# Optimization experiments

Hardware: AMD Instinct MI355X
Metric: run time of the kernel (lower is better)

## Reference

```python
import jax, jax.numpy as jnp
import numpy as np

Q_DIM = 256; KV_DIM = 256; C = 32; N_HEAD = 8; OUT_DIM = 256
B1, B2, LQ, LK = 1, 128, 256, 256


def _glorot(key, shape, gain=1.0):
    fan_in, fan_out = shape[-2], shape[-1]
    std = gain * np.sqrt(2.0 / float(fan_in + fan_out))
    dev = np.sqrt(3.0) * std
    return jax.random.uniform(key, shape, jnp.float32, -dev, dev)


def setup_inputs() -> dict:
    key = jax.random.key(0)
    ks = jax.random.split(key, 12)
    q_data = jax.random.normal(ks[0], (B1, B2, LQ, Q_DIM), jnp.float32)
    kv_data = jax.random.normal(ks[1], (B1, B2, LK, KV_DIM), jnp.float32)
    bias = jax.random.normal(ks[2], (B1, B2, N_HEAD, LQ, LK), jnp.float32)
    nonbatched_bias = jax.random.normal(ks[3], (B1, N_HEAD, LQ, LK), jnp.float32)
    # torch Linear weights are [out, in]; original init is zeros but we use
    # glorot for a non-degenerate numerical baseline.
    Wq = _glorot(ks[4], (N_HEAD * C, Q_DIM))
    Wk = _glorot(ks[5], (N_HEAD * C, KV_DIM))
    Wv = _glorot(ks[6], (N_HEAD * C, KV_DIM))
    Wg = _glorot(ks[7], (N_HEAD * C, Q_DIM))
    bg = jnp.ones((N_HEAD * C,), jnp.float32)  # bias_init=1.0
    Wo = _glorot(ks[8], (OUT_DIM, N_HEAD * C))
    bo = jnp.zeros((OUT_DIM,), jnp.float32)
    return dict(q_data=q_data, kv_data=kv_data, bias=bias,
                nonbatched_bias=nonbatched_bias, Wq=Wq, Wk=Wk, Wv=Wv,
                Wg=Wg, bg=bg, Wo=Wo, bo=bo)


def reference(q_data, kv_data, bias, nonbatched_bias, Wq, Wk, Wv, Wg, bg, Wo, bo):
    c = C
    # projections: [b1,b2,len,n_head,c]
    q = (q_data @ Wq.T).reshape(*q_data.shape[:-1], N_HEAD, c) * (c ** -0.5)
    k = (kv_data @ Wk.T).reshape(*kv_data.shape[:-1], N_HEAD, c)
    v = (kv_data @ Wv.T).reshape(*kv_data.shape[:-1], N_HEAD, c)
    # logits: [b1,b2,n_head,len_q,len_kv]
    logits = jnp.einsum('bsqhc,bskhc->bshqk', q, k)
    logits = logits + bias + nonbatched_bias[:, None]
    weights = jax.nn.softmax(logits, axis=-1)
    weighted_avg = jnp.einsum('bshqk,bskhc->bsqhc', weights, v)
    gate = jax.nn.sigmoid((q_data @ Wg.T + bg).reshape(*q_data.shape[:-1], N_HEAD, c))
    weighted_avg = weighted_avg * gate
    out = weighted_avg.reshape(*weighted_avg.shape[:-2], N_HEAD * c) @ Wo.T + bo
    return out
```

## Files before the change

kernel.cpp:

```cpp
#include <hip/hip_runtime.h>
#include <hip/hip_bf16.h>

#define NB2 128
#define LQK 256
#define DIM 256
#define NH 8
#define CC 32

typedef __bf16 bf16x8 __attribute__((ext_vector_type(8)));
typedef __bf16 bf16x4 __attribute__((ext_vector_type(4)));
typedef __bf16 bf16x2 __attribute__((ext_vector_type(2)));
typedef float f32x4 __attribute__((ext_vector_type(4)));

#define MFMA16 __builtin_amdgcn_mfma_f32_16x16x32_bf16

#define TP 72

#define NTOK ((size_t)NB2 * LQK * NH * CC)

static __device__ __forceinline__ void gload_lds16(const void* g, void* l) {
    __builtin_amdgcn_global_load_lds(
        (const __attribute__((address_space(1))) unsigned int*)g,
        (__attribute__((address_space(3))) unsigned int*)l,
        16, 0, 0);
}

__global__ __launch_bounds__(256) void k_cvt(
    const float* __restrict__ qd, const float* __restrict__ kvd,
    const float* __restrict__ Wq, const float* __restrict__ Wk,
    const float* __restrict__ Wv, const float* __restrict__ Wg,
    const float* __restrict__ Wo,
    __bf16* __restrict__ qbf, __bf16* __restrict__ kvbf,
    __bf16* __restrict__ wBF)
{
    const int b = blockIdx.x;
    if (b < 8192) {
        size_t i = ((size_t)b * 256 + threadIdx.x) * 8;
        const float* src;
        __bf16* dst;
        if (i < NTOK) { src = qd + i; dst = qbf + i; }
        else          { src = kvd + (i - NTOK); dst = kvbf + (i - NTOK); }
        f32x4 a = *(const f32x4*)src;
        f32x4 c = *(const f32x4*)(src + 4);
        bf16x8 r;
        r[0] = (__bf16)a[0]; r[1] = (__bf16)a[1]; r[2] = (__bf16)a[2]; r[3] = (__bf16)a[3];
        r[4] = (__bf16)c[0]; r[5] = (__bf16)c[1]; r[6] = (__bf16)c[2]; r[7] = (__bf16)c[3];
        *(bf16x8*)dst = r;
    } else {
        int i = ((b - 8192) * 256 + threadIdx.x) * 4;
        int mat = i >> 16;
        int off = i & 65535;
        const float* src = (mat == 0) ? Wq : (mat == 1) ? Wk : (mat == 2) ? Wv
                          : (mat == 3) ? Wg : Wo;
        f32x4 v = *(const f32x4*)(src + off);
        __bf16* d = wBF + ((size_t)mat << 16) + off;
        d[0] = (__bf16)v[0]; d[1] = (__bf16)v[1]; d[2] = (__bf16)v[2]; d[3] = (__bf16)v[3];
    }
}

__global__ __launch_bounds__(256, 2) void k_proj(
    const __bf16* __restrict__ qbf, const __bf16* __restrict__ kvbf,
    const __bf16* __restrict__ wBF, const float* __restrict__ bg,
    __bf16* __restrict__ wsq, __bf16* __restrict__ wsk,
    __bf16* __restrict__ wsvT, __bf16* __restrict__ wsg)
{
    __shared__ __bf16 At[2][128 * 64];
    __shared__ __bf16 Bt[2][128 * 64];

    const int mb = blockIdx.x, nb = blockIdx.y;
    const int t = nb >> 1;
    const __bf16* X = (t == 0 || t == 3) ? qbf : kvbf;
    const __bf16* W = wBF + ((size_t)t << 16) + (size_t)((nb & 1) * 128) * 256;

    const int tid = threadIdx.x;
    const int lane = tid & 63, w = tid >> 6;
    const int g = lane >> 4, c0 = lane & 15;
    const int mq = (w >> 1) * 64, nq = (w & 1) * 64;
    const int m0 = mb * 128;
    const int lrow = lane >> 3, lu = lane & 7;

    auto stage = [&](int buf, int kt) {
#pragma unroll
        for (int i = 0; i < 4; i++) {
            const int rr = i * 32 + w * 8 + lrow;
            const int su = lu ^ (rr & 7);
            gload_lds16(X + (size_t)(m0 + rr) * 256 + kt * 64 + su * 8,
                        &At[buf][(i * 4 + w) * 512]);
        }
#pragma unroll
        for (int i = 0; i < 4; i++) {
            const int rr = i * 32 + w * 8 + lrow;
            const int su = lu ^ (rr & 7);
            gload_lds16(W + (size_t)rr * 256 + kt * 64 + su * 8,
                        &Bt[buf][(i * 4 + w) * 512]);
        }
    };

    f32x4 acc[4][4] = {};
    stage(0, 0);
    __syncthreads();

#pragma unroll
    for (int kt = 0; kt < 4; kt++) {
        const int cur = kt & 1;
        if (kt < 3) stage(cur ^ 1, kt + 1);
#pragma unroll
        for (int ks = 0; ks < 2; ks++) {
            const int px = ((ks * 4 + g) ^ (c0 & 7)) * 8;
            bf16x8 af[4], bf_[4];
#pragma unroll
            for (int mi = 0; mi < 4; mi++)
                af[mi] = *(const bf16x8*)(&At[cur][(mq + mi * 16 + c0) * 64 + px]);
#pragma unroll
            for (int ni = 0; ni < 4; ni++)
                bf_[ni] = *(const bf16x8*)(&Bt[cur][(nq + ni * 16 + c0) * 64 + px]);
#pragma unroll
            for (int mi = 0; mi < 4; mi++)
#pragma unroll
                for (int ni = 0; ni < 4; ni++)
                    acc[mi][ni] = MFMA16(af[mi], bf_[ni], acc[mi][ni], 0, 0, 0);
        }
        __syncthreads();
    }

#pragma unroll
    for (int ni = 0; ni < 4; ni++) {
        const int nloc = (nb & 1) * 128 + nq + ni * 16 + c0;
        const int h = nloc >> 5, c = nloc & 31;
        const float bg_ = (t == 3) ? bg[nloc] : 0.0f;
#pragma unroll
        for (int mi = 0; mi < 4; mi++) {
            const int mbase = m0 + mq + mi * 16 + g * 4;
            const int b2 = mbase >> 8;
            if (t == 2) {
                bf16x4 pk;
#pragma unroll
                for (int reg = 0; reg < 4; reg++) pk[reg] = (__bf16)acc[mi][ni][reg];
                *(bf16x4*)(&wsvT[((size_t)(b2 * NH + h) * CC + c) * LQK + (mbase & 255)]) = pk;
            } else {
#pragma unroll
                for (int reg = 0; reg < 4; reg++) {
                    const int l = (mbase + reg) & 255;
                    float v = acc[mi][ni][reg];
                    size_t idx = ((size_t)(b2 * NH + h) * LQK + l) * CC + c;
                    if (t == 0)      wsq[idx] = (__bf16)(v * 0.17677669529663689f);
                    else if (t == 1) wsk[idx] = (__bf16)v;
                    else             wsg[idx] = (__bf16)(1.0f / (1.0f + __expf(-(v + bg_))));
                }
            }
        }
    }
}

__global__ __launch_bounds__(256, 3) void k_attn(
    const __bf16* __restrict__ wsq, const __bf16* __restrict__ wsk,
    const __bf16* __restrict__ wsvT, const __bf16* __restrict__ wsg,
    const float* __restrict__ bias, const float* __restrict__ nbb,
    __bf16* __restrict__ wswa)
{
    __shared__ float  Bl[2][16][256];
    __shared__ __bf16 P[4][16][TP];
    __shared__ float  lsum[2][4][16];
    __shared__ __bf16 op[2][4][16][40];

    const int tid = threadIdx.x;
    const int u0 = blockIdx.x;
    const int xcd = u0 & 7, slot = u0 >> 3;
    const int head = xcd + 8 * (slot >> 2);
    const int qt = slot & 3;
    const int b2 = head >> 3, h = head & 7;

    const int lane = tid & 63, w = tid >> 6;
    const int g = lane >> 4, kg = g * 8, c0 = lane & 15;

    const __bf16* qp = wsq + (size_t)(b2 * NH + h) * LQK * CC;
    const __bf16* kp = wsk + (size_t)(b2 * NH + h) * LQK * CC;
    const __bf16* vT = wsvT + (size_t)(b2 * NH + h) * CC * LQK;
    const __bf16* gR = wsg + (size_t)(b2 * NH + h) * LQK * CC;
    const float* npb = nbb + (size_t)h * LQK * LQK;
    const float* bblk = bias + ((size_t)(b2 * NH + h) * LQK + qt * 64) * LQK;

    auto stage = [&](int buf, int p) {
#pragma unroll
        for (int i = 0; i < 4; i++) {
            const int row = w * 4 + i;
            gload_lds16(bblk + (size_t)(p * 16 + row) * LQK + ((lane ^ row) * 4),
                        &Bl[buf][row][0]);
        }
    };

    bf16x8 kf[4], vf[4];
#pragma unroll
    for (int j = 0; j < 4; j++)
        kf[j] = *(const bf16x8*)(kp + (size_t)(w * 64 + j * 16 + c0) * CC + kg);
#pragma unroll
    for (int kt2 = 0; kt2 < 2; kt2++)
#pragma unroll
        for (int vn = 0; vn < 2; vn++)
            vf[kt2 * 2 + vn] = *(const bf16x8*)(
                vT + (size_t)(vn * 16 + c0) * LQK + w * 64 + kt2 * 32 + kg);

    const int ridx = tid * 2;
    const int rqr = ridx >> 5;
    const int rcb = ridx & 31;

    bf16x8 qfb[2];
    f32x4 nb4b[2][4];
    bf16x2 g2b[2];
    auto loadregs = [&](int buf, int p) {
        const int qglob = qt * 64 + p * 16 + c0;
        qfb[buf] = *(const bf16x8*)(qp + (size_t)qglob * CC + kg);
#pragma unroll
        for (int j = 0; j < 4; j++)
            nb4b[buf][j] = *(const f32x4*)(npb + (size_t)qglob * LQK + w * 64 + j * 16 + g * 4);
        const int qg = qt * 64 + p * 16 + rqr;
        g2b[buf] = *(const bf16x2*)(&gR[(size_t)qg * CC + rcb]);
    };

    auto compute = [&](int cur) {
        float csum = 0.0f;
#pragma unroll
        for (int j = 0; j < 4; j++) {
            f32x4 b4 = *(const f32x4*)(&Bl[cur][c0][(w * 16 + ((j * 4 + g) ^ c0)) * 4]);
            f32x4 cc;
#pragma unroll
            for (int r2 = 0; r2 < 4; r2++) cc[r2] = b4[r2] + nb4b[cur][j][r2];
            f32x4 s = MFMA16(kf[j], qfb[cur], cc, 0, 0, 0);
            bf16x4 pk;
#pragma unroll
            for (int r2 = 0; r2 < 4; r2++) {
                float e = __expf(s[r2]);
                csum += e;
                pk[r2] = (__bf16)e;
            }
            *(bf16x4*)(&P[w][c0][j * 16 + g * 4]) = pk;
        }
        csum += __shfl_xor(csum, 16);
        csum += __shfl_xor(csum, 32);
        if (lane < 16) lsum[cur][w][lane] = csum;

        f32x4 o2[2] = {};
#pragma unroll
        for (int kt2 = 0; kt2 < 2; kt2++) {
            bf16x8 pa = *(const bf16x8*)(&P[w][c0][kt2 * 32 + kg]);
#pragma unroll
            for (int vn = 0; vn < 2; vn++)
                o2[vn] = MFMA16(pa, vf[kt2 * 2 + vn], o2[vn], 0, 0, 0);
        }
#pragma unroll
        for (int vn = 0; vn < 2; vn++)
#pragma unroll
            for (int r2 = 0; r2 < 4; r2++)
                op[cur][w][g * 4 + r2][vn * 16 + c0] = (__bf16)o2[vn][r2];
    };

    auto reduce_store = [&](int p, int pb) {
        const int qg = qt * 64 + p * 16 + rqr;
        const float li = 1.0f /
            (lsum[pb][0][rqr] + lsum[pb][1][rqr] + lsum[pb][2][rqr] + lsum[pb][3][rqr]);
        float v0 = (float)op[pb][0][rqr][rcb]     + (float)op[pb][1][rqr][rcb]
                 + (float)op[pb][2][rqr][rcb]     + (float)op[pb][3][rqr][rcb];
        float v1 = (float)op[pb][0][rqr][rcb + 1] + (float)op[pb][1][rqr][rcb + 1]
                 + (float)op[pb][2][rqr][rcb + 1] + (float)op[pb][3][rqr][rcb + 1];
        v0 *= li * (float)g2b[pb][0];
        v1 *= li * (float)g2b[pb][1];
        __bf16* dst = &wswa[((size_t)(b2 * LQK + qg)) * (NH * CC) + h * CC + rcb];
        dst[0] = (__bf16)v0;
        dst[1] = (__bf16)v1;
    };

    stage(0, 0);
    loadregs(0, 0);
    __syncthreads();

    stage(1, 1); loadregs(1, 1);
    __builtin_amdgcn_sched_barrier(0);
    compute(0);
    __syncthreads();
    reduce_store(0, 0);
    stage(0, 2); loadregs(0, 2);
    __builtin_amdgcn_sched_barrier(0);
    compute(1);
    __syncthreads();
    reduce_store(1, 1);
    stage(1, 3); loadregs(1, 3);
    __builtin_amdgcn_sched_barrier(0);
    compute(0);
    __syncthreads();
    reduce_store(2, 0);
    compute(1);
    __syncthreads();
    reduce_store(3, 1);
}

__global__ __launch_bounds__(256, 2) void k_out(
    const __bf16* __restrict__ wa, const __bf16* __restrict__ wBF,
    const float* __restrict__ bo, float* __restrict__ out)
{
    __shared__ __bf16 At[2][128 * 64];
    __shared__ __bf16 Bt[2][128 * 64];

    const int mb = blockIdx.x, nb = blockIdx.y;
    const __bf16* W = wBF + ((size_t)4 << 16) + (size_t)(nb * 128) * 256;

    const int tid = threadIdx.x;
    const int lane = tid & 63, w = tid >> 6;
    const int g = lane >> 4, c0 = lane & 15;
    const int mq = (w >> 1) * 64, nq = (w & 1) * 64;
    const int m0 = mb * 128;
    const int lrow = lane >> 3, lu = lane & 7;

    auto stage = [&](int buf, int kt) {
#pragma unroll
        for (int i = 0; i < 4; i++) {
            const int rr = i * 32 + w * 8 + lrow;
            const int su = lu ^ (rr & 7);
            gload_lds16(wa + (size_t)(m0 + rr) * 256 + kt * 64 + su * 8,
                        &At[buf][(i * 4 + w) * 512]);
        }
#pragma unroll
        for (int i = 0; i < 4; i++) {
            const int rr = i * 32 + w * 8 + lrow;
            const int su = lu ^ (rr & 7);
            gload_lds16(W + (size_t)rr * 256 + kt * 64 + su * 8,
                        &Bt[buf][(i * 4 + w) * 512]);
        }
    };

    f32x4 acc[4][4] = {};
    stage(0, 0);
    __syncthreads();

#pragma unroll
    for (int kt = 0; kt < 4; kt++) {
        const int cur = kt & 1;
        if (kt < 3) stage(cur ^ 1, kt + 1);
#pragma unroll
        for (int ks = 0; ks < 2; ks++) {
            const int px = ((ks * 4 + g) ^ (c0 & 7)) * 8;
            bf16x8 af[4], bf_[4];
#pragma unroll
            for (int mi = 0; mi < 4; mi++)
                af[mi] = *(const bf16x8*)(&At[cur][(mq + mi * 16 + c0) * 64 + px]);
#pragma unroll
            for (int ni = 0; ni < 4; ni++)
                bf_[ni] = *(const bf16x8*)(&Bt[cur][(nq + ni * 16 + c0) * 64 + px]);
#pragma unroll
            for (int mi = 0; mi < 4; mi++)
#pragma unroll
                for (int ni = 0; ni < 4; ni++)
                    acc[mi][ni] = MFMA16(af[mi], bf_[ni], acc[mi][ni], 0, 0, 0);
        }
        __syncthreads();
    }

#pragma unroll
    for (int ni = 0; ni < 4; ni++) {
        const int n = nb * 128 + nq + ni * 16 + c0;
        const float bo_ = bo[n];
#pragma unroll
        for (int mi = 0; mi < 4; mi++) {
            const int mbase = m0 + mq + mi * 16 + g * 4;
#pragma unroll
            for (int reg = 0; reg < 4; reg++)
                out[(size_t)(mbase + reg) * 256 + n] = acc[mi][ni][reg] + bo_;
        }
    }
}

extern "C" void kernel_launch(void* const* d_in, const int* in_sizes, int n_in,
                              void* d_out, int out_size, void* d_ws, size_t ws_size,
                              hipStream_t stream) {
    const float* qd  = (const float*)d_in[0];
    const float* kvd = (const float*)d_in[1];
    const float* bias = (const float*)d_in[2];
    const float* nbb = (const float*)d_in[3];
    const float* Wq = (const float*)d_in[4];
    const float* Wk = (const float*)d_in[5];
    const float* Wv = (const float*)d_in[6];
    const float* Wg = (const float*)d_in[7];
    const float* bg = (const float*)d_in[8];
    const float* Wo = (const float*)d_in[9];
    const float* bo = (const float*)d_in[10];
    float* out = (float*)d_out;

    __bf16* ws = (__bf16*)d_ws;
    __bf16* wsq  = ws;
    __bf16* wsk  = wsq + NTOK;
    __bf16* wsvT = wsk + NTOK;
    __bf16* wsg  = wsvT + NTOK;
    __bf16* wBF  = wsg + NTOK;
    __bf16* qbf  = wBF + 5 * 65536;
    __bf16* kvbf = qbf + NTOK;
    __bf16* wswa = qbf;

    k_cvt<<<dim3(8512), 256, 0, stream>>>(qd, kvd, Wq, Wk, Wv, Wg, Wo,
                                          qbf, kvbf, wBF);
    k_proj<<<dim3(256, 8), 256, 0, stream>>>(qbf, kvbf, wBF, bg,
                                             wsq, wsk, wsvT, wsg);
    k_attn<<<dim3(4096), 256, 0, stream>>>(wsq, wsk, wsvT, wsg, bias, nbb, wswa);
    k_out<<<dim3(256, 2), 256, 0, stream>>>(wswa, wBF, bo, out);
}
```

Measured before the change: 155.8 us.

## Triple-buffer bias staging in attention kernel with explicit vmcnt waits

Grows the LDS bias buffer from two stages to three so the bias tile is prefetched two steps ahead. Full __syncthreads barriers are replaced by s_waitcnt vmcnt(N) plus a raw s_barrier, so later global loads stay in flight across barriers. compute now takes separate LDS-buffer and register-buffer indices. The larger LDS footprint lowers the occupancy hint from 3 to 2 blocks per CU, and the hand-counted vmcnt values must exactly match the number of outstanding loads or data races follow.

```diff
diff --git a/kernel.cpp b/kernel.cpp
--- a/kernel.cpp
+++ b/kernel.cpp
@@ -24,6 +24,12 @@
         (__attribute__((address_space(3))) unsigned int*)l,
         16, 0, 0);
 }
+
+#define WAITV(N) do { asm volatile("s_waitcnt vmcnt(" #N ")" ::: "memory"); \
+                      __builtin_amdgcn_sched_barrier(0); } while (0)
+#define BARRIER_NOV() do { asm volatile("s_waitcnt lgkmcnt(0)" ::: "memory"); \
+                           __builtin_amdgcn_s_barrier(); \
+                           __builtin_amdgcn_sched_barrier(0); } while (0)
 
 __global__ __launch_bounds__(256) void k_cvt(
     const float* __restrict__ qd, const float* __restrict__ kvd,
@@ -152,13 +158,13 @@
     }
 }
 
-__global__ __launch_bounds__(256, 3) void k_attn(
+__global__ __launch_bounds__(256, 2) void k_attn(
     const __bf16* __restrict__ wsq, const __bf16* __restrict__ wsk,
     const __bf16* __restrict__ wsvT, const __bf16* __restrict__ wsg,
     const float* __restrict__ bias, const float* __restrict__ nbb,
     __bf16* __restrict__ wswa)
 {
-    __shared__ float  Bl[2][16][256];
+    __shared__ float  Bl[3][16][256];
     __shared__ __bf16 P[4][16][TP];
     __shared__ float  lsum[2][4][16];
     __shared__ __bf16 op[2][4][16][40];
@@ -217,15 +223,15 @@
         g2b[buf] = *(const bf16x2*)(&gR[(size_t)qg * CC + rcb]);
     };
 
-    auto compute = [&](int cur) {
+    auto compute = [&](int bl, int rb) {
         float csum = 0.0f;
 #pragma unroll
         for (int j = 0; j < 4; j++) {
-            f32x4 b4 = *(const f32x4*)(&Bl[cur][c0][(w * 16 + ((j * 4 + g) ^ c0)) * 4]);
+            f32x4 b4 = *(const f32x4*)(&Bl[bl][c0][(w * 16 + ((j * 4 + g) ^ c0)) * 4]);
             f32x4 cc;
 #pragma unroll
-            for (int r2 = 0; r2 < 4; r2++) cc[r2] = b4[r2] + nb4b[cur][j][r2];
-            f32x4 s = MFMA16(kf[j], qfb[cur], cc, 0, 0, 0);
+            for (int r2 = 0; r2 < 4; r2++) cc[r2] = b4[r2] + nb4b[rb][j][r2];
+            f32x4 s = MFMA16(kf[j], qfb[rb], cc, 0, 0, 0);
             bf16x4 pk;
 #pragma unroll
             for (int r2 = 0; r2 < 4; r2++) {
@@ -237,7 +243,7 @@
         }
         csum += __shfl_xor(csum, 16);
         csum += __shfl_xor(csum, 32);
-        if (lane < 16) lsum[cur][w][lane] = csum;
+        if (lane < 16) lsum[rb][w][lane] = csum;
 
         f32x4 o2[2] = {};
 #pragma unroll
@@ -251,7 +257,7 @@
         for (int vn = 0; vn < 2; vn++)
 #pragma unroll
             for (int r2 = 0; r2 < 4; r2++)
-                op[cur][w][g * 4 + r2][vn * 16 + c0] = (__bf16)o2[vn][r2];
+                op[rb][w][g * 4 + r2][vn * 16 + c0] = (__bf16)o2[vn][r2];
     };
 
     auto reduce_store = [&](int p, int pb) {
@@ -269,26 +275,40 @@
         dst[1] = (__bf16)v1;
     };
 
+    loadregs(0, 0);
+    __builtin_amdgcn_sched_barrier(0);
     stage(0, 0);
-    loadregs(0, 0);
-    __syncthreads();
-
-    stage(1, 1); loadregs(1, 1);
-    __builtin_amdgcn_sched_barrier(0);
-    compute(0);
-    __syncthreads();
+    stage(1, 1);
+    __builtin_amdgcn_sched_barrier(0);
+
+    WAITV(4);
+    BARRIER_NOV();
+    loadregs(1, 1);
+    __builtin_amdgcn_sched_barrier(0);
+    stage(2, 2);
+    __builtin_amdgcn_sched_barrier(0);
+    compute(0, 0);
+
+    WAITV(4);
+    BARRIER_NOV();
     reduce_store(0, 0);
-    stage(0, 2); loadregs(0, 2);
-    __builtin_amdgcn_sched_barrier(0);
-    compute(1);
-    __syncthreads();
+    loadregs(0, 2);
+    __builtin_amdgcn_sched_barrier(0);
+    stage(0, 3);
+    __builtin_amdgcn_sched_barrier(0);
+    compute(1, 1);
+
+    WAITV(4);
+    BARRIER_NOV();
     reduce_store(1, 1);
-    stage(1, 3); loadregs(1, 3);
-    __builtin_amdgcn_sched_barrier(0);
-    compute(0);
-    __syncthreads();
+    loadregs(1, 3);
+    __builtin_amdgcn_sched_barrier(0);
+    compute(2, 0);
+
+    WAITV(0);
+    BARRIER_NOV();
     reduce_store(2, 0);
-    compute(1);
+    compute(0, 1);
     __syncthreads();
     reduce_store(3, 1);
 }
```

After: 160.2 us. +2.8%, slower.
